# Kernel optimization log

Measured on AMD Instinct MI355X. Metric: run time of the kernel, lower is better.

## Reference

```python
import jax, jax.numpy as jnp
import numpy as np

EMBED_DIM = 1024
HEAD_DIM = 64
BATCH = 2
SEQ = 4096


def setup_inputs() -> dict:
    key = jax.random.key(0)
    kx, kq, kk, kv = jax.random.split(key, 4)
    x = jax.random.normal(kx, (BATCH, SEQ, EMBED_DIM), dtype=jnp.float32)
    # nn.Linear(embedding_dim, head_dim, bias=False) weights, stored as [in, out]
    s = 1.0 / np.sqrt(EMBED_DIM)
    Wq = jax.random.uniform(kq, (EMBED_DIM, HEAD_DIM), jnp.float32, -s, s)
    Wk = jax.random.uniform(kk, (EMBED_DIM, HEAD_DIM), jnp.float32, -s, s)
    Wv = jax.random.uniform(kv, (EMBED_DIM, HEAD_DIM), jnp.float32, -s, s)
    return {"x": x, "Wq": Wq, "Wk": Wk, "Wv": Wv}


def reference(x, Wq, Wk, Wv):
    # x: [B, S, E]
    Q = x @ Wq  # [B, S, D]
    K = x @ Wk
    V = x @ Wv
    seq_len = Q.shape[1]
    head_dim = Q.shape[2]
    scores = jnp.einsum('bsd,btd->bst', Q, K) / jnp.sqrt(jnp.float32(head_dim))
    # Original adds a mask that is 1.0 on the causal (lower-tri) positions and
    # -inf elsewhere (tril(ones) with zeros replaced by -inf). The +1 on allowed
    # positions is a uniform row shift, but we keep it for bitwise faithfulness.
    causal = jnp.tril(jnp.ones((seq_len, seq_len), dtype=scores.dtype))
    mask = jnp.where(causal == 0, -jnp.inf, causal)
    scores = scores + mask  # [B, S, S]
    attn = jax.nn.softmax(scores, axis=-1)
    return jnp.einsum('bst,btd->bsd', attn, V)  # [B, S, D]
```

## Files before the change

### kernel.cpp

```cpp
#include <hip/hip_runtime.h>
#include <hip/hip_bf16.h>


typedef short short8 __attribute__((ext_vector_type(8)));
typedef float f32x2 __attribute__((ext_vector_type(2)));
typedef float f32x4 __attribute__((ext_vector_type(4)));
typedef float f32x16 __attribute__((ext_vector_type(16)));
typedef unsigned int uint4e __attribute__((ext_vector_type(4)));
typedef unsigned short ushort4e __attribute__((ext_vector_type(4)));

#define NEGINF (-3.0e38f)
#define SCQ 0.18033688011112042f

static __device__ __forceinline__ unsigned short f2bf(float f) {
  __hip_bfloat16 h = __float2bfloat16(f);
  return __builtin_bit_cast(unsigned short, h);
}
static __device__ __forceinline__ f32x16 mfma32(short8 a, short8 b, f32x16 c) {
  return __builtin_amdgcn_mfma_f32_32x32x16_bf16(a, b, c, 0, 0, 0);
}

__global__ __launch_bounds__(256) void wprep_kernel(
    const float* __restrict__ Wq, const float* __restrict__ Wk,
    const float* __restrict__ Wv, unsigned short* __restrict__ Wt) {
  int w = blockIdx.x >> 3;
  int kc = blockIdx.x & 7;
  int k0 = kc * 128;
  const float* W = (w == 0) ? Wq : ((w == 1) ? Wk : Wv);
  float sc = (w == 0) ? SCQ : 1.0f;

  __shared__ unsigned short lt[128][66];
#pragma unroll
  for (int i = 0; i < 32; ++i) {
    int e = i * 256 + threadIdx.x;
    int k = e >> 6, n = e & 63;
    lt[k][n] = f2bf(W[(size_t)(k0 + k) * 64 + n] * sc);
  }
  __syncthreads();
#pragma unroll
  for (int i = 0; i < 32; ++i) {
    int e = i * 256 + threadIdx.x;
    int n = e >> 7, k = e & 127;
    Wt[(size_t)(w * 64 + n) * 1024 + k0 + k] = lt[k][n];
  }
}

__global__ __launch_bounds__(512) void qkv_proj_kernel(
    const float* __restrict__ x, const unsigned short* __restrict__ Wt,
    unsigned short* __restrict__ Qb, unsigned short* __restrict__ Kb,
    unsigned short* __restrict__ Vt) {
  int tid = threadIdx.x;
  int lane = tid & 63;
  int wv = tid >> 6;
  int rt = wv >> 2;
  int cg = wv & 3;
  int r = lane & 15;
  int hi = lane >> 4;
  int sbase = blockIdx.x * 32;

  __shared__ alignas(16) unsigned short xs[2][32][40];
  __shared__ alignas(16) unsigned short wsl[2][192][40];

  int xrow = tid >> 4;
  int xcol = (tid & 15) * 2;
  int p1 = tid;
  int p2 = tid + 512;
  const float* xg = x + (size_t)(sbase + xrow) * 1024 + xcol;

  f32x4 acc[3];
#pragma unroll
  for (int t = 0; t < 3; ++t)
#pragma unroll
    for (int i = 0; i < 4; ++i) acc[t][i] = 0.f;

  {
    f32x2 xv = *(const f32x2*)(xg);
    unsigned int pk = (unsigned int)f2bf(xv[0]) | ((unsigned int)f2bf(xv[1]) << 16);
    *(unsigned int*)&xs[0][xrow][xcol] = pk;
    short8 wva = *(const short8*)(Wt + (size_t)(p1 >> 2) * 1024 + (p1 & 3) * 8);
    *(short8*)&wsl[0][p1 >> 2][(p1 & 3) * 8] = wva;
    if (tid < 256) {
      short8 wvb = *(const short8*)(Wt + (size_t)(p2 >> 2) * 1024 + (p2 & 3) * 8);
      *(short8*)&wsl[0][p2 >> 2][(p2 & 3) * 8] = wvb;
    }
  }
  __syncthreads();

  for (int c = 0; c < 32; ++c) {
    int cur = c & 1;
    bool has_next = (c + 1) < 32;
    f32x2 xv;
    short8 wva, wvb;
    if (has_next) {
      int k0 = (c + 1) * 32;
      xv = *(const f32x2*)(xg + k0);
      wva = *(const short8*)(Wt + (size_t)(p1 >> 2) * 1024 + k0 + (p1 & 3) * 8);
      if (tid < 256)
        wvb = *(const short8*)(Wt + (size_t)(p2 >> 2) * 1024 + k0 + (p2 & 3) * 8);
    }
    short8 af = *(const short8*)&xs[cur][rt * 16 + r][hi * 8];
#pragma unroll
    for (int tt = 0; tt < 3; ++tt) {
      short8 bf = *(const short8*)&wsl[cur][(cg * 3 + tt) * 16 + r][hi * 8];
      acc[tt] = __builtin_amdgcn_mfma_f32_16x16x32_bf16(af, bf, acc[tt], 0, 0, 0);
    }
    if (has_next) {
      int nb = cur ^ 1;
      unsigned int pk = (unsigned int)f2bf(xv[0]) | ((unsigned int)f2bf(xv[1]) << 16);
      *(unsigned int*)&xs[nb][xrow][xcol] = pk;
      *(short8*)&wsl[nb][p1 >> 2][(p1 & 3) * 8] = wva;
      if (tid < 256) *(short8*)&wsl[nb][p2 >> 2][(p2 & 3) * 8] = wvb;
    }
    __syncthreads();
  }

  int lr = rt * 16 + hi * 4;
#pragma unroll
  for (int tt = 0; tt < 3; ++tt) {
    int gt = cg * 3 + tt;
    if (gt < 8) {
      unsigned short* dst = (gt < 4) ? Qb : Kb;
      int col = (gt & 3) * 16 + r;
#pragma unroll
      for (int v = 0; v < 4; ++v)
        dst[(size_t)(sbase + lr + v) * 64 + col] = f2bf(acc[tt][v]);
    } else {
      int d = (gt - 8) * 16 + r;
      ushort4e pk;
#pragma unroll
      for (int v = 0; v < 4; ++v) pk[v] = f2bf(acc[tt][v]);
      int bidx = sbase >> 12;
      int so = (sbase & 4095) + lr;
      *(ushort4e*)(Vt + ((size_t)(bidx * 64 + d)) * 4096 + so) = pk;
    }
  }
}

__global__ __launch_bounds__(256, 2) void attn_kernel(
    const unsigned short* __restrict__ Qb, const unsigned short* __restrict__ Kb,
    const unsigned short* __restrict__ Vt, float* __restrict__ Opart,
    float* __restrict__ Mpart, float* __restrict__ Lpart) {
  int bid = blockIdx.x;
  int q = 127 - (bid >> 3);
  int b = (bid >> 2) & 1;
  int hh = bid & 3;
  int lane = threadIdx.x & 63;
  int p = threadIdx.x >> 6;
  int g = hh * 4 + p;
  int ql = lane & 31;
  int h = lane >> 5;
  int sbase = q * 32;

  __shared__ float sm[4][32];
  __shared__ float sl[4][32];
  __shared__ alignas(16) float Op[4][32][68];

  const unsigned short* Qp = Qb + ((size_t)(b * 4096 + sbase + ql)) * 64 + h * 8;
  short8 qf0 = *(const short8*)(Qp);
  short8 qf1 = *(const short8*)(Qp + 16);
  short8 qf2 = *(const short8*)(Qp + 32);
  short8 qf3 = *(const short8*)(Qp + 48);

  f32x16 o0, o1;
#pragma unroll
  for (int i = 0; i < 16; ++i) { o0[i] = 0.f; o1[i] = 0.f; }
  float m = NEGINF, l = 0.f;

  int npairs = (q + 2) >> 1;
  const unsigned short* Kbb = Kb + (size_t)b * 4096 * 64;
  const unsigned short* Vbb = Vt + ((size_t)(b * 64 + ql)) * 4096 + h * 8;

  short8 k0a, k0b, k0c, k0d, k1a, k1b, k1c, k1d;
  {
    const unsigned short* Kp = Kbb + (size_t)(g * 64 + ql) * 64 + h * 8;
    k0a = *(const short8*)(Kp);
    k0b = *(const short8*)(Kp + 16);
    k0c = *(const short8*)(Kp + 32);
    k0d = *(const short8*)(Kp + 48);
    k1a = *(const short8*)(Kp + 2048);
    k1b = *(const short8*)(Kp + 2048 + 16);
    k1c = *(const short8*)(Kp + 2048 + 32);
    k1d = *(const short8*)(Kp + 2048 + 48);
  }

  for (int j = g; j < npairs; j += 16) {
    int kbase = j * 64;
    const unsigned short* Vp = Vbb + kbase;
    short8 vf0 = *(const short8*)(Vp);
    short8 vf1 = *(const short8*)(Vp + 16);
    short8 vf2 = *(const short8*)(Vp + 32);
    short8 vf3 = *(const short8*)(Vp + 48);
    short8 vg0 = *(const short8*)(Vp + 32 * 4096);
    short8 vg1 = *(const short8*)(Vp + 32 * 4096 + 16);
    short8 vg2 = *(const short8*)(Vp + 32 * 4096 + 32);
    short8 vg3 = *(const short8*)(Vp + 32 * 4096 + 48);

    f32x16 st0, st1;
#pragma unroll
    for (int i = 0; i < 16; ++i) { st0[i] = 0.f; st1[i] = 0.f; }
    __builtin_amdgcn_s_setprio(1);
    st0 = mfma32(k0a, qf0, st0);
    st0 = mfma32(k0b, qf1, st0);
    st0 = mfma32(k0c, qf2, st0);
    st0 = mfma32(k0d, qf3, st0);
    st1 = mfma32(k1a, qf0, st1);
    st1 = mfma32(k1b, qf1, st1);
    st1 = mfma32(k1c, qf2, st1);
    st1 = mfma32(k1d, qf3, st1);
    __builtin_amdgcn_s_setprio(0);

    if (j + 16 < npairs) {
      const unsigned short* Kp = Kbb + (size_t)((j + 16) * 64 + ql) * 64 + h * 8;
      k0a = *(const short8*)(Kp);
      k0b = *(const short8*)(Kp + 16);
      k0c = *(const short8*)(Kp + 32);
      k0d = *(const short8*)(Kp + 48);
      k1a = *(const short8*)(Kp + 2048);
      k1b = *(const short8*)(Kp + 2048 + 16);
      k1c = *(const short8*)(Kp + 2048 + 32);
      k1d = *(const short8*)(Kp + 2048 + 48);
    }

    if (2 * j == q) {
#pragma unroll
      for (int rg = 0; rg < 16; ++rg) {
        int kvl = (rg & 3) + 8 * (rg >> 2) + 4 * h;
        if (kvl > ql) st0[rg] = NEGINF;
        st1[rg] = NEGINF;
      }
    } else if (2 * j + 1 == q) {
#pragma unroll
      for (int rg = 0; rg < 16; ++rg) {
        int kvl = (rg & 3) + 8 * (rg >> 2) + 4 * h;
        if (kvl > ql) st1[rg] = NEGINF;
      }
    }

    float mx[16];
#pragma unroll
    for (int i = 0; i < 16; ++i) mx[i] = fmaxf(st0[i], st1[i]);
#pragma unroll
    for (int s = 8; s >= 1; s >>= 1)
#pragma unroll
      for (int i = 0; i < s; ++i) mx[i] = fmaxf(mx[i], mx[i + s]);
    float tm = fmaxf(mx[0], __shfl_xor(mx[0], 32));
    float nm = fmaxf(m, tm);
    float alpha = exp2f(m - nm);
#pragma unroll
    for (int i = 0; i < 16; ++i) {
      st0[i] = exp2f(st0[i] - nm);
      st1[i] = exp2f(st1[i] - nm);
    }
    float sv[16];
#pragma unroll
    for (int i = 0; i < 16; ++i) sv[i] = st0[i] + st1[i];
#pragma unroll
    for (int s = 8; s >= 1; s >>= 1)
#pragma unroll
      for (int i = 0; i < s; ++i) sv[i] += sv[i + s];
    float sum = sv[0] + __shfl_xor(sv[0], 32);
    l = l * alpha + sum;
    m = nm;
#pragma unroll
    for (int i = 0; i < 16; ++i) { o0[i] *= alpha; o1[i] *= alpha; }

    unsigned int pw0[8], pw1[8], sw0[8], sw1[8];
#pragma unroll
    for (int t = 0; t < 8; ++t) {
      pw0[t] = (unsigned int)f2bf(st0[2 * t]) | ((unsigned int)f2bf(st0[2 * t + 1]) << 16);
      pw1[t] = (unsigned int)f2bf(st1[2 * t]) | ((unsigned int)f2bf(st1[2 * t + 1]) << 16);
    }
#pragma unroll
    for (int t = 0; t < 8; ++t) {
      sw0[t] = __shfl_xor(pw0[t], 32);
      sw1[t] = __shfl_xor(pw1[t], 32);
    }
    uint4e bw0 = {h ? sw0[2] : pw0[0], h ? sw0[3] : pw0[1], h ? pw0[2] : sw0[0], h ? pw0[3] : sw0[1]};
    uint4e bw1 = {h ? sw0[6] : pw0[4], h ? sw0[7] : pw0[5], h ? pw0[6] : sw0[4], h ? pw0[7] : sw0[5]};
    uint4e bw2 = {h ? sw1[2] : pw1[0], h ? sw1[3] : pw1[1], h ? pw1[2] : sw1[0], h ? pw1[3] : sw1[1]};
    uint4e bw3 = {h ? sw1[6] : pw1[4], h ? sw1[7] : pw1[5], h ? pw1[6] : sw1[4], h ? pw1[7] : sw1[5]};
    short8 pb0 = __builtin_bit_cast(short8, bw0);
    short8 pb1 = __builtin_bit_cast(short8, bw1);
    short8 pb2 = __builtin_bit_cast(short8, bw2);
    short8 pb3 = __builtin_bit_cast(short8, bw3);

    __builtin_amdgcn_s_setprio(1);
    o0 = mfma32(vf0, pb0, o0);
    o0 = mfma32(vf1, pb1, o0);
    o0 = mfma32(vf2, pb2, o0);
    o0 = mfma32(vf3, pb3, o0);
    o1 = mfma32(vg0, pb0, o1);
    o1 = mfma32(vg1, pb1, o1);
    o1 = mfma32(vg2, pb2, o1);
    o1 = mfma32(vg3, pb3, o1);
    __builtin_amdgcn_s_setprio(0);
  }

  if (h == 0) sm[p][ql] = m;
  __syncthreads();
  float gm = sm[0][ql];
#pragma unroll
  for (int i = 1; i < 4; ++i) gm = fmaxf(gm, sm[i][ql]);
  float alpha = exp2f(m - gm);
  if (h == 0) sl[p][ql] = alpha * l;
  float* Ob = &Op[p][ql][0];
#pragma unroll
  for (int u = 0; u < 4; ++u) {
    f32x4 w0 = {alpha * o0[4 * u], alpha * o0[4 * u + 1], alpha * o0[4 * u + 2], alpha * o0[4 * u + 3]};
    *(f32x4*)(Ob + u * 8 + h * 4) = w0;
    f32x4 w1 = {alpha * o1[4 * u], alpha * o1[4 * u + 1], alpha * o1[4 * u + 2], alpha * o1[4 * u + 3]};
    *(f32x4*)(Ob + 32 + u * 8 + h * 4) = w1;
  }
  __syncthreads();

  float* Od = Opart + (size_t)bid * 2048;
#pragma unroll
  for (int i = 0; i < 2; ++i) {
    int task = threadIdx.x + i * 256;
    int row = task >> 4;
    int c4 = (task & 15) * 4;
    f32x4 accv = *(const f32x4*)(&Op[0][row][c4]);
#pragma unroll
    for (int pp = 1; pp < 4; ++pp) accv += *(const f32x4*)(&Op[pp][row][c4]);
    *(f32x4*)(Od + row * 64 + c4) = accv;
  }
  if (threadIdx.x < 32) {
    int row = threadIdx.x;
    float gmv = fmaxf(fmaxf(sm[0][row], sm[1][row]), fmaxf(sm[2][row], sm[3][row]));
    Mpart[(size_t)bid * 32 + row] = gmv;
    Lpart[(size_t)bid * 32 + row] = sl[0][row] + sl[1][row] + sl[2][row] + sl[3][row];
  }
}

__global__ __launch_bounds__(256) void combine_kernel(
    const float* __restrict__ Opart, const float* __restrict__ Mpart,
    const float* __restrict__ Lpart, float* __restrict__ out) {
  int gid = blockIdx.x * 256 + threadIdx.x;
  int c4 = (gid & 15) * 4;
  int row = gid >> 4;
  int r = row & 31;
  int qg = row >> 5;
  int b = qg >> 7, q = qg & 127;
  int base = (127 - q) * 8 + b * 4;

  float mm[4];
  float gm = NEGINF;
#pragma unroll
  for (int i = 0; i < 4; ++i) {
    mm[i] = Mpart[(size_t)(base + i) * 32 + r];
    gm = fmaxf(gm, mm[i]);
  }
  float L = 0.f;
  f32x4 o = {0.f, 0.f, 0.f, 0.f};
#pragma unroll
  for (int i = 0; i < 4; ++i) {
    float e = exp2f(mm[i] - gm);
    L += e * Lpart[(size_t)(base + i) * 32 + r];
    f32x4 ov = *(const f32x4*)(Opart + (size_t)(base + i) * 2048 + r * 64 + c4);
    o += e * ov;
  }
  float invl = 1.0f / L;
  f32x4 res = {o[0] * invl, o[1] * invl, o[2] * invl, o[3] * invl};
  *(f32x4*)(out + (size_t)row * 64 + c4) = res;
}

extern "C" void kernel_launch(void* const* d_in, const int* in_sizes, int n_in,
                              void* d_out, int out_size, void* d_ws, size_t ws_size,
                              hipStream_t stream) {
  const float* x  = (const float*)d_in[0];
  const float* Wq = (const float*)d_in[1];
  const float* Wk = (const float*)d_in[2];
  const float* Wv = (const float*)d_in[3];
  float* out = (float*)d_out;

  if (ws_size < 12189696) return;

  char* ws = (char*)d_ws;
  unsigned short* Wt = (unsigned short*)(ws + 0);
  unsigned short* Qb = (unsigned short*)(ws + 393216);
  unsigned short* Kb = (unsigned short*)(ws + 1441792);
  unsigned short* Vt = (unsigned short*)(ws + 2490368);
  float* Opart = (float*)(ws + 3538944);
  float* Mpart = (float*)(ws + 11927552);
  float* Lpart = (float*)(ws + 12058624);

  wprep_kernel<<<24, 256, 0, stream>>>(Wq, Wk, Wv, Wt);
  qkv_proj_kernel<<<256, 512, 0, stream>>>(x, Wt, Qb, Kb, Vt);
  attn_kernel<<<1024, 256, 0, stream>>>(Qb, Kb, Vt, Opart, Mpart, Lpart);
  combine_kernel<<<512, 256, 0, stream>>>(Opart, Mpart, Lpart, out);
}
```

Before: 125.3 us.

## Double attention split-KV partitions and retile QKV projection to 16-row blocks

The attention kernel now splits each query tile's KV range across 8 blocks (32 wave groups) instead of 4, doubling grid size and raising the occupancy hint to 4 blocks per CU. The combine kernel merges 8 partials per row, and the workspace for partial outputs grows to match. The QKV projection switches to 256-thread blocks covering 16 rows with a 64-wide K chunk, giving more blocks and fewer loop iterations. The goal is better load balance and latency hiding on the causal triangle, at the cost of more partial-output traffic and combine work, plus register pressure under the tighter launch bound.

```diff
diff --git a/kernel.cpp b/kernel.cpp
--- a/kernel.cpp
+++ b/kernel.cpp
@@ -3,7 +3,6 @@
 
 
 typedef short short8 __attribute__((ext_vector_type(8)));
-typedef float f32x2 __attribute__((ext_vector_type(2)));
 typedef float f32x4 __attribute__((ext_vector_type(4)));
 typedef float f32x16 __attribute__((ext_vector_type(16)));
 typedef unsigned int uint4e __attribute__((ext_vector_type(4)));
@@ -45,26 +44,22 @@
   }
 }
 
-__global__ __launch_bounds__(512) void qkv_proj_kernel(
+__global__ __launch_bounds__(256, 2) void qkv_proj_kernel(
     const float* __restrict__ x, const unsigned short* __restrict__ Wt,
     unsigned short* __restrict__ Qb, unsigned short* __restrict__ Kb,
     unsigned short* __restrict__ Vt) {
   int tid = threadIdx.x;
   int lane = tid & 63;
-  int wv = tid >> 6;
-  int rt = wv >> 2;
-  int cg = wv & 3;
+  int w = tid >> 6;
   int r = lane & 15;
   int hi = lane >> 4;
-  int sbase = blockIdx.x * 32;
-
-  __shared__ alignas(16) unsigned short xs[2][32][40];
-  __shared__ alignas(16) unsigned short wsl[2][192][40];
+  int sbase = blockIdx.x * 16;
+
+  __shared__ alignas(16) unsigned short xs[2][16][72];
+  __shared__ alignas(16) unsigned short wsh[2][192][72];
 
   int xrow = tid >> 4;
-  int xcol = (tid & 15) * 2;
-  int p1 = tid;
-  int p2 = tid + 512;
+  int xcol = (tid & 15) * 4;
   const float* xg = x + (size_t)(sbase + xrow) * 1024 + xcol;
 
   f32x4 acc[3];
@@ -74,50 +69,63 @@
     for (int i = 0; i < 4; ++i) acc[t][i] = 0.f;
 
   {
-    f32x2 xv = *(const f32x2*)(xg);
-    unsigned int pk = (unsigned int)f2bf(xv[0]) | ((unsigned int)f2bf(xv[1]) << 16);
-    *(unsigned int*)&xs[0][xrow][xcol] = pk;
-    short8 wva = *(const short8*)(Wt + (size_t)(p1 >> 2) * 1024 + (p1 & 3) * 8);
-    *(short8*)&wsl[0][p1 >> 2][(p1 & 3) * 8] = wva;
-    if (tid < 256) {
-      short8 wvb = *(const short8*)(Wt + (size_t)(p2 >> 2) * 1024 + (p2 & 3) * 8);
-      *(short8*)&wsl[0][p2 >> 2][(p2 & 3) * 8] = wvb;
+    f32x4 xv = *(const f32x4*)(xg);
+    ushort4e xp;
+#pragma unroll
+    for (int j = 0; j < 4; ++j) xp[j] = f2bf(xv[j]);
+    *(ushort4e*)&xs[0][xrow][xcol] = xp;
+#pragma unroll
+    for (int i = 0; i < 6; ++i) {
+      int p = tid + 256 * i;
+      short8 wv = *(const short8*)(Wt + (size_t)(p >> 3) * 1024 + (p & 7) * 8);
+      *(short8*)&wsh[0][p >> 3][(p & 7) * 8] = wv;
     }
   }
   __syncthreads();
 
-  for (int c = 0; c < 32; ++c) {
+  for (int c = 0; c < 16; ++c) {
     int cur = c & 1;
-    bool has_next = (c + 1) < 32;
-    f32x2 xv;
-    short8 wva, wvb;
+    bool has_next = (c + 1) < 16;
+    f32x4 xv;
+    short8 wv[6];
     if (has_next) {
-      int k0 = (c + 1) * 32;
-      xv = *(const f32x2*)(xg + k0);
-      wva = *(const short8*)(Wt + (size_t)(p1 >> 2) * 1024 + k0 + (p1 & 3) * 8);
-      if (tid < 256)
-        wvb = *(const short8*)(Wt + (size_t)(p2 >> 2) * 1024 + k0 + (p2 & 3) * 8);
-    }
-    short8 af = *(const short8*)&xs[cur][rt * 16 + r][hi * 8];
+      int k0 = (c + 1) * 64;
+      xv = *(const f32x4*)(xg + k0);
+#pragma unroll
+      for (int i = 0; i < 6; ++i) {
+        int p = tid + 256 * i;
+        wv[i] = *(const short8*)(Wt + (size_t)(p >> 3) * 1024 + k0 + (p & 7) * 8);
+      }
+    }
+    short8 af0 = *(const short8*)&xs[cur][r][hi * 8];
+    short8 af1 = *(const short8*)&xs[cur][r][32 + hi * 8];
 #pragma unroll
     for (int tt = 0; tt < 3; ++tt) {
-      short8 bf = *(const short8*)&wsl[cur][(cg * 3 + tt) * 16 + r][hi * 8];
-      acc[tt] = __builtin_amdgcn_mfma_f32_16x16x32_bf16(af, bf, acc[tt], 0, 0, 0);
+      const unsigned short* bp = &wsh[cur][w * 48 + tt * 16 + r][hi * 8];
+      short8 bf0 = *(const short8*)bp;
+      short8 bf1 = *(const short8*)(bp + 32);
+      acc[tt] = __builtin_amdgcn_mfma_f32_16x16x32_bf16(af0, bf0, acc[tt], 0, 0, 0);
+      acc[tt] = __builtin_amdgcn_mfma_f32_16x16x32_bf16(af1, bf1, acc[tt], 0, 0, 0);
     }
     if (has_next) {
       int nb = cur ^ 1;
-      unsigned int pk = (unsigned int)f2bf(xv[0]) | ((unsigned int)f2bf(xv[1]) << 16);
-      *(unsigned int*)&xs[nb][xrow][xcol] = pk;
-      *(short8*)&wsl[nb][p1 >> 2][(p1 & 3) * 8] = wva;
-      if (tid < 256) *(short8*)&wsl[nb][p2 >> 2][(p2 & 3) * 8] = wvb;
+      ushort4e xp;
+#pragma unroll
+      for (int j = 0; j < 4; ++j) xp[j] = f2bf(xv[j]);
+      *(ushort4e*)&xs[nb][xrow][xcol] = xp;
+#pragma unroll
+      for (int i = 0; i < 6; ++i) {
+        int p = tid + 256 * i;
+        *(short8*)&wsh[nb][p >> 3][(p & 7) * 8] = wv[i];
+      }
     }
     __syncthreads();
   }
 
-  int lr = rt * 16 + hi * 4;
+  int lr = hi * 4;
 #pragma unroll
   for (int tt = 0; tt < 3; ++tt) {
-    int gt = cg * 3 + tt;
+    int gt = w * 3 + tt;
     if (gt < 8) {
       unsigned short* dst = (gt < 4) ? Qb : Kb;
       int col = (gt & 3) * 16 + r;
@@ -136,14 +144,14 @@
   }
 }
 
-__global__ __launch_bounds__(256, 2) void attn_kernel(
+__global__ __launch_bounds__(256, 4) void attn_kernel(
     const unsigned short* __restrict__ Qb, const unsigned short* __restrict__ Kb,
     const unsigned short* __restrict__ Vt, float* __restrict__ Opart,
     float* __restrict__ Mpart, float* __restrict__ Lpart) {
   int bid = blockIdx.x;
-  int q = 127 - (bid >> 3);
-  int b = (bid >> 2) & 1;
-  int hh = bid & 3;
+  int q = 127 - (bid >> 4);
+  int b = (bid >> 3) & 1;
+  int hh = bid & 7;
   int lane = threadIdx.x & 63;
   int p = threadIdx.x >> 6;
   int g = hh * 4 + p;
@@ -171,7 +179,7 @@
   const unsigned short* Vbb = Vt + ((size_t)(b * 64 + ql)) * 4096 + h * 8;
 
   short8 k0a, k0b, k0c, k0d, k1a, k1b, k1c, k1d;
-  {
+  if (g < npairs) {
     const unsigned short* Kp = Kbb + (size_t)(g * 64 + ql) * 64 + h * 8;
     k0a = *(const short8*)(Kp);
     k0b = *(const short8*)(Kp + 16);
@@ -183,7 +191,7 @@
     k1d = *(const short8*)(Kp + 2048 + 48);
   }
 
-  for (int j = g; j < npairs; j += 16) {
+  for (int j = g; j < npairs; j += 32) {
     int kbase = j * 64;
     const unsigned short* Vp = Vbb + kbase;
     short8 vf0 = *(const short8*)(Vp);
@@ -209,8 +217,8 @@
     st1 = mfma32(k1d, qf3, st1);
     __builtin_amdgcn_s_setprio(0);
 
-    if (j + 16 < npairs) {
-      const unsigned short* Kp = Kbb + (size_t)((j + 16) * 64 + ql) * 64 + h * 8;
+    if (j + 32 < npairs) {
+      const unsigned short* Kp = Kbb + (size_t)((j + 32) * 64 + ql) * 64 + h * 8;
       k0a = *(const short8*)(Kp);
       k0b = *(const short8*)(Kp + 16);
       k0c = *(const short8*)(Kp + 32);
@@ -341,19 +349,19 @@
   int r = row & 31;
   int qg = row >> 5;
   int b = qg >> 7, q = qg & 127;
-  int base = (127 - q) * 8 + b * 4;
-
-  float mm[4];
+  int base = (127 - q) * 16 + b * 8;
+
+  float mm[8];
   float gm = NEGINF;
 #pragma unroll
-  for (int i = 0; i < 4; ++i) {
+  for (int i = 0; i < 8; ++i) {
     mm[i] = Mpart[(size_t)(base + i) * 32 + r];
     gm = fmaxf(gm, mm[i]);
   }
   float L = 0.f;
   f32x4 o = {0.f, 0.f, 0.f, 0.f};
 #pragma unroll
-  for (int i = 0; i < 4; ++i) {
+  for (int i = 0; i < 8; ++i) {
     float e = exp2f(mm[i] - gm);
     L += e * Lpart[(size_t)(base + i) * 32 + r];
     f32x4 ov = *(const f32x4*)(Opart + (size_t)(base + i) * 2048 + r * 64 + c4);
@@ -373,7 +381,7 @@
   const float* Wv = (const float*)d_in[3];
   float* out = (float*)d_out;
 
-  if (ws_size < 12189696) return;
+  if (ws_size < 20840448) return;
 
   char* ws = (char*)d_ws;
   unsigned short* Wt = (unsigned short*)(ws + 0);
@@ -381,11 +389,11 @@
   unsigned short* Kb = (unsigned short*)(ws + 1441792);
   unsigned short* Vt = (unsigned short*)(ws + 2490368);
   float* Opart = (float*)(ws + 3538944);
-  float* Mpart = (float*)(ws + 11927552);
-  float* Lpart = (float*)(ws + 12058624);
+  float* Mpart = (float*)(ws + 20316160);
+  float* Lpart = (float*)(ws + 20578304);
 
   wprep_kernel<<<24, 256, 0, stream>>>(Wq, Wk, Wv, Wt);
-  qkv_proj_kernel<<<256, 512, 0, stream>>>(x, Wt, Qb, Kb, Vt);
-  attn_kernel<<<1024, 256, 0, stream>>>(Qb, Kb, Vt, Opart, Mpart, Lpart);
+  qkv_proj_kernel<<<512, 256, 0, stream>>>(x, Wt, Qb, Kb, Vt);
+  attn_kernel<<<2048, 256, 0, stream>>>(Qb, Kb, Vt, Opart, Mpart, Lpart);
   combine_kernel<<<512, 256, 0, stream>>>(Opart, Mpart, Lpart, out);
 }
```

Measured after the change: 158.1 us. 26.2% more time.
